# Performance work log

Measured on AMD Instinct MI355X. Metric: run time of the kernel, lower is better.

The kernel has to match this reference:

```python
import jax, jax.numpy as jnp
import numpy as np

T = 5          # Newton-Schulz iterations
EPS = 1e-05


def reference(X):
    # X: (B, C, L); training-mode IterNorm whitening with num_groups=1
    B, C, L = X.shape
    x = jnp.transpose(X, (1, 0, 2)).reshape(C, -1)        # (d, m)
    d, m = x.shape
    mean = jnp.mean(x, axis=-1, keepdims=True)
    xc = x - mean                                         # (d, m)
    I = jnp.eye(d, dtype=X.dtype)
    Sigma = I * EPS + (xc @ xc.T) * (1.0 / m)             # (d, d)
    rTr = 1.0 / jnp.trace(Sigma)                          # scalar
    Sigma_N = Sigma * rTr
    P = I
    for _ in range(T):
        P = 1.5 * P - 0.5 * (P @ P @ P) @ Sigma_N
    wm = P * jnp.sqrt(rTr)                                # whitening matrix
    xn = wm @ xc                                          # (d, m)
    Xn = jnp.transpose(xn.reshape(C, B, L), (1, 0, 2))
    return Xn


def setup_inputs() -> dict:
    key = jax.random.key(0)
    X = jax.random.normal(key, (32, 64, 8192), dtype=jnp.float32)
    return {"X": X}
```

## Files before the change

kernel.cpp:

```cpp
#include <hip/hip_runtime.h>
#include <math.h>

#define L_DIM   8192
#define NCH     64
#define M_TOT_F 262144.0f
#define EPS_F   1e-5f
#define GTPB    4
#define ATPB    4

typedef float f32x4 __attribute__((ext_vector_type(4)));
typedef short bf16x8 __attribute__((ext_vector_type(8)));

union U8 { unsigned u[4]; bf16x8 v; };

__device__ __forceinline__ void cvt2(float f0, float f1, unsigned& h, unsigned& l) {
    unsigned u0 = __float_as_uint(f0), u1 = __float_as_uint(f1);
    h = (u0 >> 16) | (u1 & 0xFFFF0000u);
    float r0 = f0 - __uint_as_float(u0 & 0xFFFF0000u);
    float r1 = f1 - __uint_as_float(u1 & 0xFFFF0000u);
    l = (__float_as_uint(r0) >> 16) | (__float_as_uint(r1) & 0xFFFF0000u);
}

__device__ __forceinline__ void split16(float v, unsigned short& h, unsigned short& l) {
    unsigned u = __float_as_uint(v);
    h = (unsigned short)(u >> 16);
    float r = v - __uint_as_float(u & 0xFFFF0000u);
    l = (unsigned short)(__float_as_uint(r) >> 16);
}

__device__ __forceinline__ f32x4 mfma16(bf16x8 a, bf16x8 b, f32x4 c) {
    return __builtin_amdgcn_mfma_f32_16x16x32_bf16(a, b, c, 0, 0, 0);
}

__device__ __forceinline__ f32x4 fzero() {
    f32x4 z; z[0] = 0.f; z[1] = 0.f; z[2] = 0.f; z[3] = 0.f; return z;
}

__global__ __launch_bounds__(256) void gram_kernel(const float* __restrict__ X,
                                                   float* __restrict__ P) {
    __shared__ __align__(16) unsigned short hfrag[2][4096];
    __shared__ __align__(16) unsigned short lfrag[2][4096];
    const int tid  = threadIdx.x;
    const int w    = tid >> 6;
    const int lane = tid & 63;
    const int m    = lane & 15;
    const int q    = lane >> 4;
    const int row  = 16 * w + m;

    f32x4 acc1[4], acc2[4];
#pragma unroll
    for (int nb = 0; nb < 4; ++nb) { acc1[nb] = fzero(); acc2[nb] = fzero(); }
    float sacc = 0.f;

    const int tile0 = blockIdx.x * GTPB;
    float4 v[GTPB][4];
#pragma unroll
    for (int t = 0; t < GTPB; ++t) {
        int tt = tile0 + t;
        const float* src = X + ((size_t)((tt >> 7) * NCH + row)) * L_DIM + ((tt & 127) << 6) + 8 * q;
        v[t][0] = *(const float4*)(src);
        v[t][1] = *(const float4*)(src + 4);
        v[t][2] = *(const float4*)(src + 32);
        v[t][3] = *(const float4*)(src + 36);
    }

#pragma unroll
    for (int t = 0; t < GTPB; ++t) {
        const int p = t & 1;
#pragma unroll
        for (int i = 0; i < 4; ++i) sacc += v[t][i].x + v[t][i].y + v[t][i].z + v[t][i].w;

        bf16x8 Ah[2], Al[2];
#pragma unroll
        for (int k = 0; k < 2; ++k) {
            U8 H, L;
            cvt2(v[t][2 * k].x,     v[t][2 * k].y,     H.u[0], L.u[0]);
            cvt2(v[t][2 * k].z,     v[t][2 * k].w,     H.u[1], L.u[1]);
            cvt2(v[t][2 * k + 1].x, v[t][2 * k + 1].y, H.u[2], L.u[2]);
            cvt2(v[t][2 * k + 1].z, v[t][2 * k + 1].w, H.u[3], L.u[3]);
            Ah[k] = H.v; Al[k] = L.v;
            int chunk = ((w * 2 + k) * 4 + q) * 16 + m;
            *(bf16x8*)&hfrag[p][chunk * 8] = H.v;
            *(bf16x8*)&lfrag[p][chunk * 8] = L.v;
        }
        __syncthreads();

#pragma unroll
        for (int k = 0; k < 2; ++k)
#pragma unroll
            for (int nb = 0; nb < 4; ++nb) {
                int chunk = ((nb * 2 + k) * 4 + q) * 16 + m;
                bf16x8 bh = *(const bf16x8*)&hfrag[p][chunk * 8];
                bf16x8 bl = *(const bf16x8*)&lfrag[p][chunk * 8];
                acc1[nb] = mfma16(Ah[k], bh, acc1[nb]);
                acc2[nb] = mfma16(Ah[k], bl, acc2[nb]);
            }
    }

    float* base = P + (size_t)blockIdx.x * 8256;
#pragma unroll
    for (int nb = 0; nb < 4; ++nb)
#pragma unroll
        for (int r = 0; r < 4; ++r) {
            int grow = 16 * w + 4 * q + r;
            int gcol = 16 * nb + m;
            base[grow * 64 + gcol]        = acc1[nb][r];
            base[4096 + grow * 64 + gcol] = acc2[nb][r];
        }
    sacc += __shfl_xor(sacc, 16);
    sacc += __shfl_xor(sacc, 32);
    if (q == 0) base[8192 + row] = sacc;
}

__global__ __launch_bounds__(256) void reduce_kernel(const float* __restrict__ P,
                                                     float* __restrict__ ws) {
    const int tid = threadIdx.x;
    const int w = tid >> 6, lane = tid & 63;
    const int e0 = blockIdx.x * 64;
    float a0 = 0.f, a1 = 0.f, a2 = 0.f, a3 = 0.f;
#pragma unroll 8
    for (int i = 0; i < 64; ++i) {
        const float* p = P + (size_t)(w * 256 + 4 * i) * 8256 + e0 + lane;
        a0 += p[0];
        a1 += p[8256];
        a2 += p[2 * 8256];
        a3 += p[3 * 8256];
    }
    float a = (a0 + a1) + (a2 + a3);
    __shared__ float red[4][64];
    red[w][lane] = a;
    __syncthreads();
    if (w == 0)
        ws[e0 + lane] = red[0][lane] + red[1][lane] + red[2][lane] + red[3][lane];
}

__device__ __forceinline__ void mm_core8(f32x4* acc,
                                         const unsigned short* Xh, const unsigned short* Xl,
                                         const unsigned short* Yh, const unsigned short* Yl,
                                         int rg, int nbb, int m, int q) {
#pragma unroll
    for (int k0 = 0; k0 < 64; k0 += 32) {
        bf16x8 xh = *(const bf16x8*)&Xh[(16 * rg + m) * 72 + k0 + 8 * q];
        bf16x8 xl = *(const bf16x8*)&Xl[(16 * rg + m) * 72 + k0 + 8 * q];
#pragma unroll
        for (int j = 0; j < 2; ++j) {
            int nb = nbb + j;
            bf16x8 yh = *(const bf16x8*)&Yh[(16 * nb + m) * 72 + k0 + 8 * q];
            bf16x8 yl = *(const bf16x8*)&Yl[(16 * nb + m) * 72 + k0 + 8 * q];
            acc[j] = mfma16(xh, yh, acc[j]);
            acc[j] = mfma16(xh, yl, acc[j]);
            acc[j] = mfma16(xl, yh, acc[j]);
        }
    }
}

__device__ __forceinline__ void mm_pl8(unsigned short* Dh, unsigned short* Dl,
                                       const unsigned short* Xh, const unsigned short* Xl,
                                       const unsigned short* Yh, const unsigned short* Yl,
                                       int rg, int nbb, int m, int q) {
    f32x4 acc[2];
    acc[0] = fzero(); acc[1] = fzero();
    mm_core8(acc, Xh, Xl, Yh, Yl, rg, nbb, m, q);
#pragma unroll
    for (int j = 0; j < 2; ++j)
#pragma unroll
        for (int r = 0; r < 4; ++r) {
            int row = 16 * rg + 4 * q + r, col = 16 * (nbb + j) + m;
            unsigned short h, l;
            split16(acc[j][r], h, l);
            Dh[row * 72 + col] = h;
            Dl[row * 72 + col] = l;
        }
}

__global__ __launch_bounds__(512) void ns_kernel(float* __restrict__ ws) {
    __shared__ __align__(16) float Pf[64 * 68];
    __shared__ __align__(16) unsigned short Ph[64 * 72], Pl[64 * 72];
    __shared__ __align__(16) unsigned short Sh[64 * 72], Sl[64 * 72];
    __shared__ __align__(16) unsigned short T1h[64 * 72], T1l[64 * 72];
    __shared__ __align__(16) unsigned short T2h[64 * 72], T2l[64 * 72];
    __shared__ float mu[64];
    __shared__ float scal[2];

    const int tid = threadIdx.x;
    const int w8 = tid >> 6, lane = tid & 63;
    const int m = lane & 15, q = lane >> 4;
    const int rg = w8 >> 1, nbb = (w8 & 1) << 1;
    const float inv_m = 1.0f / M_TOT_F;

    if (tid < 64) mu[tid] = ws[8192 + tid] * inv_m;
    __syncthreads();

    if (tid < 64) {
        int e = tid * 65;
        float g  = (ws[e] + 2.0f * ws[4096 + e]) * inv_m;
        float sd = g - mu[tid] * mu[tid] + EPS_F;
#pragma unroll
        for (int off = 32; off >= 1; off >>= 1) sd += __shfl_xor(sd, off);
        if (tid == 0) { scal[0] = 1.0f / sd; scal[1] = sqrtf(1.0f / sd); }
    }
    __syncthreads();
    const float rTr = scal[0];

    for (int e = tid; e < 4096; e += 512) {
        int i = e >> 6, j = e & 63;
        float g   = (ws[e] + ws[4096 + e] + ws[4096 + (j << 6) + i]) * inv_m;
        float sig = g - mu[i] * mu[j] + ((i == j) ? EPS_F : 0.f);
        float sn  = sig * rTr;
        unsigned short h, l;
        split16(sn, h, l);
        Sh[i * 72 + j] = h; Sl[i * 72 + j] = l;
        float pv = ((i == j) ? 1.5f : 0.f) - 0.5f * sn;
        Pf[i * 68 + j] = pv;
        split16(pv, h, l);
        Ph[i * 72 + j] = h; Pl[i * 72 + j] = l;
    }
    __syncthreads();

    for (int it = 0; it < 4; ++it) {
        mm_pl8(T1h, T1l, Ph, Pl, Ph, Pl, rg, nbb, m, q);
        __syncthreads();
        mm_pl8(T2h, T2l, T1h, T1l, Ph, Pl, rg, nbb, m, q);
        __syncthreads();
        f32x4 acc[2];
        acc[0] = fzero(); acc[1] = fzero();
        mm_core8(acc, T2h, T2l, Sh, Sl, rg, nbb, m, q);
#pragma unroll
        for (int j = 0; j < 2; ++j)
#pragma unroll
            for (int r = 0; r < 4; ++r) {
                int row = 16 * rg + 4 * q + r, col = 16 * (nbb + j) + m;
                int idx = row * 68 + col;
                float pv = 1.5f * Pf[idx] - 0.5f * acc[j][r];
                Pf[idx] = pv;
                unsigned short h, l;
                split16(pv, h, l);
                Ph[row * 72 + col] = h;
                Pl[row * 72 + col] = l;
            }
        __syncthreads();
    }

    const float s = scal[1];
    unsigned short* hp = (unsigned short*)ws;
    unsigned short* lp = hp + 4096;
    for (int e = tid; e < 4096; e += 512) {
        int i = e >> 6, j = e & 63;
        float v = Pf[i * 68 + j] * s;
        unsigned short h, l;
        split16(v, h, l);
        hp[e] = h;
        lp[e] = l;
    }
    if (tid < 64) {
        float a = 0.f;
#pragma unroll 8
        for (int k = 0; k < 64; ++k) a += Pf[tid * 68 + k] * mu[k];
        ws[8256 + tid] = -a * s;
    }
}

__global__ __launch_bounds__(256) void apply_kernel(const float* __restrict__ X,
                                                    float* __restrict__ Y,
                                                    const float* __restrict__ ws) {
    __shared__ __align__(16) unsigned short hplane[2][4096];
    __shared__ __align__(16) unsigned short lplane[2][4096];
    const int tid  = threadIdx.x;
    const int w    = tid >> 6;
    const int lane = tid & 63;
    const int m    = lane & 15;
    const int q    = lane >> 4;
    const int cp   = tid & 31;
    const int lg   = tid >> 5;

    const unsigned short* hp = (const unsigned short*)ws;
    const unsigned short* lp = hp + 4096;
    bf16x8 Ah[2], Al[2];
#pragma unroll
    for (int kk = 0; kk < 2; ++kk) {
        Ah[kk] = *(const bf16x8*)&hp[(16 * w + m) * 64 + 32 * kk + 8 * q];
        Al[kk] = *(const bf16x8*)&lp[(16 * w + m) * 64 + 32 * kk + 8 * q];
    }
    const float4 bias4 = *(const float4*)&ws[8256 + 16 * w + 4 * q];

    float4 va[ATPB][2], vb[ATPB][2];
#pragma unroll
    for (int t = 0; t < ATPB; ++t) {
        int tile = blockIdx.x * ATPB + t;
        const float* xb = X + (size_t)(tile >> 7) * (NCH * L_DIM) + ((tile & 127) << 6)
                          + (size_t)(2 * cp) * L_DIM + 4 * lg;
#pragma unroll
        for (int ss = 0; ss < 2; ++ss) {
            va[t][ss] = *(const float4*)(xb + 32 * ss);
            vb[t][ss] = *(const float4*)(xb + 32 * ss + L_DIM);
        }
    }

#pragma unroll
    for (int t = 0; t < ATPB; ++t) {
        int tile = blockIdx.x * ATPB + t;
        int bidx = tile >> 7;
        int l0   = (tile & 127) << 6;
        const int p = t & 1;
        unsigned* hw2 = (unsigned*)hplane[p];
        unsigned* lw2 = (unsigned*)lplane[p];

#pragma unroll
        for (int ss = 0; ss < 2; ++ss) {
            float fa[4], fb[4];
            *(float4*)fa = va[t][ss];
            *(float4*)fb = vb[t][ss];
#pragma unroll
            for (int i = 0; i < 4; ++i) {
                int l = 4 * lg + 32 * ss + i;
                unsigned h, lo2;
                cvt2(fa[i], fb[i], h, lo2);
                int widx = l * 32 + (((cp >> 2) ^ (l & 7)) << 2) + (cp & 3);
                hw2[widx] = h;
                lw2[widx] = lo2;
            }
        }
        __syncthreads();

        f32x4 acc[4];
#pragma unroll
        for (int nb = 0; nb < 4; ++nb) {
            acc[nb][0] = bias4.x; acc[nb][1] = bias4.y;
            acc[nb][2] = bias4.z; acc[nb][3] = bias4.w;
        }
#pragma unroll
        for (int kk = 0; kk < 2; ++kk)
#pragma unroll
            for (int nb = 0; nb < 4; ++nb) {
                int l = 16 * nb + m;
                int saddr = l * 64 + ((((4 * kk + q) ^ (l & 7))) << 3);
                bf16x8 bh = *(const bf16x8*)&hplane[p][saddr];
                bf16x8 bl = *(const bf16x8*)&lplane[p][saddr];
                acc[nb] = mfma16(Ah[kk], bh, acc[nb]);
                acc[nb] = mfma16(Ah[kk], bl, acc[nb]);
                acc[nb] = mfma16(Al[kk], bh, acc[nb]);
            }

#pragma unroll
        for (int nb = 0; nb < 4; ++nb)
#pragma unroll
            for (int rr = 0; rr < 4; ++rr)
                Y[((size_t)bidx * NCH + 16 * w + 4 * q + rr) * L_DIM + l0 + 16 * nb + m] = acc[nb][rr];
    }
}

extern "C" void kernel_launch(void* const* d_in, const int* in_sizes, int n_in,
                              void* d_out, int out_size, void* d_ws, size_t ws_size,
                              hipStream_t stream) {
    const float* X = (const float*)d_in[0];
    float* Y  = (float*)d_out;
    float* ws = (float*)d_ws;
    float* scratch = (float*)d_out;

    hipLaunchKernelGGL(gram_kernel,   dim3(1024), dim3(256), 0, stream, X, scratch);
    hipLaunchKernelGGL(reduce_kernel, dim3(129),  dim3(256), 0, stream, scratch, ws);
    hipLaunchKernelGGL(ns_kernel,     dim3(1),    dim3(512), 0, stream, ws);
    hipLaunchKernelGGL(apply_kernel,  dim3(1024), dim3(256), 0, stream, X, Y, ws);
}
```

Baseline: 153.8 us.

## Replace partial-sum reduce kernel with atomic accumulation and pipeline gram loads

The gram kernel now processes 8 tiles per block over 512 blocks. It prefetches the next tile's global loads into a 4-slot register ring while the current tile is converted and multiplied. Partial Gram and sum results are accumulated directly into the workspace with float atomicAdd after a memset, which removes the separate reduce kernel and its scratch write and read traffic. The cost is 512-way atomic contention on 8256 addresses and a nondeterministic summation order.

```diff
diff --git a/kernel.cpp b/kernel.cpp
--- a/kernel.cpp
+++ b/kernel.cpp
@@ -5,7 +5,8 @@
 #define NCH     64
 #define M_TOT_F 262144.0f
 #define EPS_F   1e-5f
-#define GTPB    4
+#define GBLK    512
+#define GTPB    8
 #define ATPB    4
 
 typedef float f32x4 __attribute__((ext_vector_type(4)));
@@ -37,7 +38,7 @@
 }
 
 __global__ __launch_bounds__(256) void gram_kernel(const float* __restrict__ X,
-                                                   float* __restrict__ P) {
+                                                   float* __restrict__ ws) {
     __shared__ __align__(16) unsigned short hfrag[2][4096];
     __shared__ __align__(16) unsigned short lfrag[2][4096];
     const int tid  = threadIdx.x;
@@ -53,36 +54,43 @@
     float sacc = 0.f;
 
     const int tile0 = blockIdx.x * GTPB;
-    float4 v[GTPB][4];
+    float4 v[4][4];
+
+#define LDT(slot, tt)  {                                                                   \
+        const float* src_ = X + ((size_t)(((tt) >> 7) * NCH + row)) * L_DIM                \
+                              + (((tt) & 127) << 6) + 8 * q;                               \
+        v[slot][0] = *(const float4*)(src_);                                               \
+        v[slot][1] = *(const float4*)(src_ + 4);                                           \
+        v[slot][2] = *(const float4*)(src_ + 32);                                          \
+        v[slot][3] = *(const float4*)(src_ + 36);                                          \
+    }
+
+#pragma unroll
+    for (int t = 0; t < 4; ++t) LDT(t, tile0 + t)
+
 #pragma unroll
     for (int t = 0; t < GTPB; ++t) {
-        int tt = tile0 + t;
-        const float* src = X + ((size_t)((tt >> 7) * NCH + row)) * L_DIM + ((tt & 127) << 6) + 8 * q;
-        v[t][0] = *(const float4*)(src);
-        v[t][1] = *(const float4*)(src + 4);
-        v[t][2] = *(const float4*)(src + 32);
-        v[t][3] = *(const float4*)(src + 36);
-    }
-
-#pragma unroll
-    for (int t = 0; t < GTPB; ++t) {
-        const int p = t & 1;
-#pragma unroll
-        for (int i = 0; i < 4; ++i) sacc += v[t][i].x + v[t][i].y + v[t][i].z + v[t][i].w;
+        const int slot = t & 3;
+        const int p    = t & 1;
+#pragma unroll
+        for (int i = 0; i < 4; ++i)
+            sacc += v[slot][i].x + v[slot][i].y + v[slot][i].z + v[slot][i].w;
 
         bf16x8 Ah[2], Al[2];
 #pragma unroll
         for (int k = 0; k < 2; ++k) {
             U8 H, L;
-            cvt2(v[t][2 * k].x,     v[t][2 * k].y,     H.u[0], L.u[0]);
-            cvt2(v[t][2 * k].z,     v[t][2 * k].w,     H.u[1], L.u[1]);
-            cvt2(v[t][2 * k + 1].x, v[t][2 * k + 1].y, H.u[2], L.u[2]);
-            cvt2(v[t][2 * k + 1].z, v[t][2 * k + 1].w, H.u[3], L.u[3]);
+            cvt2(v[slot][2 * k].x,     v[slot][2 * k].y,     H.u[0], L.u[0]);
+            cvt2(v[slot][2 * k].z,     v[slot][2 * k].w,     H.u[1], L.u[1]);
+            cvt2(v[slot][2 * k + 1].x, v[slot][2 * k + 1].y, H.u[2], L.u[2]);
+            cvt2(v[slot][2 * k + 1].z, v[slot][2 * k + 1].w, H.u[3], L.u[3]);
             Ah[k] = H.v; Al[k] = L.v;
             int chunk = ((w * 2 + k) * 4 + q) * 16 + m;
             *(bf16x8*)&hfrag[p][chunk * 8] = H.v;
             *(bf16x8*)&lfrag[p][chunk * 8] = L.v;
         }
+
+        if (t + 4 < GTPB) LDT(slot, tile0 + t + 4)
         __syncthreads();
 
 #pragma unroll
@@ -96,42 +104,20 @@
                 acc2[nb] = mfma16(Ah[k], bl, acc2[nb]);
             }
     }
-
-    float* base = P + (size_t)blockIdx.x * 8256;
+#undef LDT
+
 #pragma unroll
     for (int nb = 0; nb < 4; ++nb)
 #pragma unroll
         for (int r = 0; r < 4; ++r) {
             int grow = 16 * w + 4 * q + r;
             int gcol = 16 * nb + m;
-            base[grow * 64 + gcol]        = acc1[nb][r];
-            base[4096 + grow * 64 + gcol] = acc2[nb][r];
+            atomicAdd(&ws[grow * 64 + gcol],        acc1[nb][r]);
+            atomicAdd(&ws[4096 + grow * 64 + gcol], acc2[nb][r]);
         }
     sacc += __shfl_xor(sacc, 16);
     sacc += __shfl_xor(sacc, 32);
-    if (q == 0) base[8192 + row] = sacc;
-}
-
-__global__ __launch_bounds__(256) void reduce_kernel(const float* __restrict__ P,
-                                                     float* __restrict__ ws) {
-    const int tid = threadIdx.x;
-    const int w = tid >> 6, lane = tid & 63;
-    const int e0 = blockIdx.x * 64;
-    float a0 = 0.f, a1 = 0.f, a2 = 0.f, a3 = 0.f;
-#pragma unroll 8
-    for (int i = 0; i < 64; ++i) {
-        const float* p = P + (size_t)(w * 256 + 4 * i) * 8256 + e0 + lane;
-        a0 += p[0];
-        a1 += p[8256];
-        a2 += p[2 * 8256];
-        a3 += p[3 * 8256];
-    }
-    float a = (a0 + a1) + (a2 + a3);
-    __shared__ float red[4][64];
-    red[w][lane] = a;
-    __syncthreads();
-    if (w == 0)
-        ws[e0 + lane] = red[0][lane] + red[1][lane] + red[2][lane] + red[3][lane];
+    if (q == 0) atomicAdd(&ws[8192 + row], sacc);
 }
 
 __device__ __forceinline__ void mm_core8(f32x4* acc,
@@ -355,10 +341,9 @@
     const float* X = (const float*)d_in[0];
     float* Y  = (float*)d_out;
     float* ws = (float*)d_ws;
-    float* scratch = (float*)d_out;
-
-    hipLaunchKernelGGL(gram_kernel,   dim3(1024), dim3(256), 0, stream, X, scratch);
-    hipLaunchKernelGGL(reduce_kernel, dim3(129),  dim3(256), 0, stream, scratch, ws);
-    hipLaunchKernelGGL(ns_kernel,     dim3(1),    dim3(512), 0, stream, ws);
-    hipLaunchKernelGGL(apply_kernel,  dim3(1024), dim3(256), 0, stream, X, Y, ws);
-}
+
+    hipMemsetAsync(ws, 0, 8256 * sizeof(float), stream);
+    hipLaunchKernelGGL(gram_kernel,  dim3(GBLK), dim3(256), 0, stream, X, ws);
+    hipLaunchKernelGGL(ns_kernel,    dim3(1),    dim3(512), 0, stream, ws);
+    hipLaunchKernelGGL(apply_kernel, dim3(1024), dim3(256), 0, stream, X, Y, ws);
+}
```

Result: slower. 159.9 us (+3.9%).

## Fold split-precision Gram partials in-block to halve scratch traffic and split reduction

Applied to the files above, without the earlier changes.

The gram kernel now combines the high and low-residual accumulators, plus the transposed low-cross term, inside each block through shared memory. Each block therefore writes one 64x64 partial instead of two, which halves the per-block scratch writes and the reduce kernel's reads. The reduction is split into two halves written to separate buffers, which the NS kernel sums. This adds an extra shared-memory pass and two barriers per gram block and changes the floating-point summation order.

```diff
diff --git a/kernel.cpp b/kernel.cpp
--- a/kernel.cpp
+++ b/kernel.cpp
@@ -7,6 +7,7 @@
 #define EPS_F   1e-5f
 #define GTPB    4
 #define ATPB    4
+#define PSTRIDE 4224
 
 typedef float f32x4 __attribute__((ext_vector_type(4)));
 typedef short bf16x8 __attribute__((ext_vector_type(8)));
@@ -38,8 +39,11 @@
 
 __global__ __launch_bounds__(256) void gram_kernel(const float* __restrict__ X,
                                                    float* __restrict__ P) {
-    __shared__ __align__(16) unsigned short hfrag[2][4096];
-    __shared__ __align__(16) unsigned short lfrag[2][4096];
+    __shared__ __align__(16) unsigned char arena[32768];
+    unsigned short (*hfrag)[4096] = (unsigned short(*)[4096])(arena);
+    unsigned short (*lfrag)[4096] = (unsigned short(*)[4096])(arena + 16384);
+    float* fg2 = (float*)arena;
+
     const int tid  = threadIdx.x;
     const int w    = tid >> 6;
     const int lane = tid & 63;
@@ -97,41 +101,57 @@
             }
     }
 
-    float* base = P + (size_t)blockIdx.x * 8256;
+    __syncthreads();
 #pragma unroll
     for (int nb = 0; nb < 4; ++nb)
 #pragma unroll
         for (int r = 0; r < 4; ++r) {
             int grow = 16 * w + 4 * q + r;
             int gcol = 16 * nb + m;
-            base[grow * 64 + gcol]        = acc1[nb][r];
-            base[4096 + grow * 64 + gcol] = acc2[nb][r];
+            fg2[grow * 65 + gcol] = acc2[nb][r];
+        }
+    __syncthreads();
+
+    float* base = P + (size_t)blockIdx.x * PSTRIDE;
+#pragma unroll
+    for (int nb = 0; nb < 4; ++nb)
+#pragma unroll
+        for (int r = 0; r < 4; ++r) {
+            int grow = 16 * w + 4 * q + r;
+            int gcol = 16 * nb + m;
+            base[grow * 64 + gcol] = acc1[nb][r] + acc2[nb][r] + fg2[gcol * 65 + grow];
         }
     sacc += __shfl_xor(sacc, 16);
     sacc += __shfl_xor(sacc, 32);
-    if (q == 0) base[8192 + row] = sacc;
+    if (q == 0) base[4096 + row] = sacc;
 }
 
 __global__ __launch_bounds__(256) void reduce_kernel(const float* __restrict__ P,
-                                                     float* __restrict__ ws) {
+                                                     float* __restrict__ H0,
+                                                     float* __restrict__ H1) {
     const int tid = threadIdx.x;
     const int w = tid >> 6, lane = tid & 63;
-    const int e0 = blockIdx.x * 64;
+    const int s = blockIdx.x % 65;
+    const int h = blockIdx.x / 65;
+    const int e0 = s * 64;
+    const float* base = P + (size_t)(h * 512 + w * 128) * PSTRIDE + e0 + lane;
     float a0 = 0.f, a1 = 0.f, a2 = 0.f, a3 = 0.f;
 #pragma unroll 8
-    for (int i = 0; i < 64; ++i) {
-        const float* p = P + (size_t)(w * 256 + 4 * i) * 8256 + e0 + lane;
+    for (int i = 0; i < 32; ++i) {
+        const float* p = base + (size_t)(4 * i) * PSTRIDE;
         a0 += p[0];
-        a1 += p[8256];
-        a2 += p[2 * 8256];
-        a3 += p[3 * 8256];
+        a1 += p[PSTRIDE];
+        a2 += p[2 * PSTRIDE];
+        a3 += p[3 * PSTRIDE];
     }
     float a = (a0 + a1) + (a2 + a3);
     __shared__ float red[4][64];
     red[w][lane] = a;
     __syncthreads();
-    if (w == 0)
-        ws[e0 + lane] = red[0][lane] + red[1][lane] + red[2][lane] + red[3][lane];
+    if (w == 0) {
+        float r = red[0][lane] + red[1][lane] + red[2][lane] + red[3][lane];
+        (h ? H1 : H0)[e0 + lane] = r;
+    }
 }
 
 __device__ __forceinline__ void mm_core8(f32x4* acc,
@@ -173,7 +193,8 @@
         }
 }
 
-__global__ __launch_bounds__(512) void ns_kernel(float* __restrict__ ws) {
+__global__ __launch_bounds__(512) void ns_kernel(float* __restrict__ ws,
+                                                 const float* __restrict__ H1) {
     __shared__ __align__(16) float Pf[64 * 68];
     __shared__ __align__(16) unsigned short Ph[64 * 72], Pl[64 * 72];
     __shared__ __align__(16) unsigned short Sh[64 * 72], Sl[64 * 72];
@@ -188,12 +209,12 @@
     const int rg = w8 >> 1, nbb = (w8 & 1) << 1;
     const float inv_m = 1.0f / M_TOT_F;
 
-    if (tid < 64) mu[tid] = ws[8192 + tid] * inv_m;
+    if (tid < 64) mu[tid] = (ws[4096 + tid] + H1[4096 + tid]) * inv_m;
     __syncthreads();
 
     if (tid < 64) {
         int e = tid * 65;
-        float g  = (ws[e] + 2.0f * ws[4096 + e]) * inv_m;
+        float g  = (ws[e] + H1[e]) * inv_m;
         float sd = g - mu[tid] * mu[tid] + EPS_F;
 #pragma unroll
         for (int off = 32; off >= 1; off >>= 1) sd += __shfl_xor(sd, off);
@@ -204,7 +225,7 @@
 
     for (int e = tid; e < 4096; e += 512) {
         int i = e >> 6, j = e & 63;
-        float g   = (ws[e] + ws[4096 + e] + ws[4096 + (j << 6) + i]) * inv_m;
+        float g   = (ws[e] + H1[e]) * inv_m;
         float sig = g - mu[i] * mu[j] + ((i == j) ? EPS_F : 0.f);
         float sn  = sig * rTr;
         unsigned short h, l;
@@ -356,9 +377,10 @@
     float* Y  = (float*)d_out;
     float* ws = (float*)d_ws;
     float* scratch = (float*)d_out;
+    float* H1 = scratch + (size_t)1024 * PSTRIDE;
 
     hipLaunchKernelGGL(gram_kernel,   dim3(1024), dim3(256), 0, stream, X, scratch);
-    hipLaunchKernelGGL(reduce_kernel, dim3(129),  dim3(256), 0, stream, scratch, ws);
-    hipLaunchKernelGGL(ns_kernel,     dim3(1),    dim3(512), 0, stream, ws);
+    hipLaunchKernelGGL(reduce_kernel, dim3(130),  dim3(256), 0, stream, scratch, ws, H1);
+    hipLaunchKernelGGL(ns_kernel,     dim3(1),    dim3(512), 0, stream, ws, H1);
     hipLaunchKernelGGL(apply_kernel,  dim3(1024), dim3(256), 0, stream, X, Y, ws);
 }
```

Measured after the change: 147.0 us. 1.05x faster.
